# Kernel tuning notes

Hardware: AMD Instinct MI355X
Metric: run time of the kernel (lower is better)

Reference implementation:

```python
import jax, jax.numpy as jnp
import numpy as np
import math

IN_DIM = 512
LR_MUL = 1.0
SCALE = (1.0 / math.sqrt(IN_DIM)) * LR_MUL  # EqualLinear runtime weight scale


def setup_inputs() -> dict:
    key = jax.random.key(0)
    k1, k2 = jax.random.split(key)
    x = jax.random.normal(k1, (256, 18, 18, 512), dtype=jnp.float32)  # [B, n_out, n_layers, in_dim]
    W = jax.random.normal(k2, (18, 512, 512), dtype=jnp.float32)      # [n_out, out_dim, in_dim]
    b = jnp.zeros((18, 512), dtype=jnp.float32)                        # [n_out, out_dim], bias_init=0
    idx = jnp.arange(18, dtype=jnp.int32)                              # n_indx
    return {"x": x, "W": W, "b": b, "idx": idx}


def reference(x, W, b, idx):
    # Fused equivalent of the nested loops: for each direction i, apply
    # EqualLinear_i to slices x[:, i, j, :] for j in idx, writing results back.
    x_sel = x[:, :, idx, :]                                    # [B, O, J, D_in]
    y = jnp.einsum('koji,odi->kojd', x_sel, W) * SCALE         # [B, O, J, D_out]
    y = y + (b * LR_MUL)[None, :, None, :]
    return x.at[:, :, idx, :].set(y)
```

## Files before the change

kernel.cpp:

```cpp
#include <hip/hip_runtime.h>
#include <hip/hip_bf16.h>


typedef __bf16  bf16x8  __attribute__((ext_vector_type(8)));
typedef float   floatx4 __attribute__((ext_vector_type(4)));

#define O_DIM 18
#define J_DIM 18
#define KB    256
#define C_DIM 512
#define BM    128
#define BN    128
#define BK    32
#define NK    (C_DIM / BK)
#define LDSS  40

__device__ __forceinline__ __bf16 f2bf(float f) { return (__bf16)f; }

__device__ __forceinline__ void barrier_lds() {
    __builtin_amdgcn_s_waitcnt(0xc07f);
    __builtin_amdgcn_s_barrier();
}

__global__ __launch_bounds__(256, 2)
void dirnet_gemm(const float* __restrict__ x, const float* __restrict__ W,
                 const float* __restrict__ bias, const int* __restrict__ idx,
                 float* __restrict__ out)
{
    const int id   = blockIdx.x;
    const int xcd  = id & 7;
    const int slot = id >> 3;
    const int nt   = slot & 3;
    const int g    = (slot >> 2) * 8 + xcd;
    const int mt   = g & 1;
    const int jo   = g >> 1;
    const int j    = jo % J_DIM;
    const int o    = jo / J_DIM;
    const int jj   = idx[j];

    __shared__ __bf16 As[BM * LDSS];
    __shared__ __bf16 Bs[BN * LDSS];

    const int tid  = threadIdx.x;
    const int srow = tid >> 2;
    const int scol = (tid & 3) << 3;

    const float* xp = x + ((size_t)((mt * BM + srow) * O_DIM + o) * J_DIM + jj) * C_DIM + scol;
    const size_t xRS = (size_t)64 * O_DIM * J_DIM * C_DIM;
    const float* wp = W + ((size_t)(o * C_DIM + nt * BN + srow)) * C_DIM + scol;
    const size_t wRS = (size_t)64 * C_DIM;

    const int lane = tid & 63;
    const int wv   = tid >> 6;
    const int mOff = (wv & 1) * 64;
    const int nOff = (wv >> 1) * 64;
    const int lrow = lane & 15;
    const int lk   = (lane >> 4) << 3;

    floatx4 acc[4][4] = {};
    float4 pa[2][2][2];
    float4 pb[2][2];

    #pragma unroll
    for (int p = 0; p < 2; ++p) {
        pb[p][0] = *(const float4*)(wp + p * wRS);
        pb[p][1] = *(const float4*)(wp + p * wRS + 4);
    }
    #pragma unroll
    for (int p = 0; p < 2; ++p) {
        pa[0][p][0] = *(const float4*)(xp + p * xRS);
        pa[0][p][1] = *(const float4*)(xp + p * xRS + 4);
    }
    #pragma unroll
    for (int p = 0; p < 2; ++p) {
        pa[1][p][0] = *(const float4*)(xp + p * xRS + BK);
        pa[1][p][1] = *(const float4*)(xp + p * xRS + BK + 4);
    }

    #pragma unroll
    for (int t = 0; t < NK; ++t) {
        const int s = t & 1;

        bf16x8 sa[2], sb[2];
        #pragma unroll
        for (int p = 0; p < 2; ++p) {
            sa[p][0]=f2bf(pa[s][p][0].x); sa[p][1]=f2bf(pa[s][p][0].y);
            sa[p][2]=f2bf(pa[s][p][0].z); sa[p][3]=f2bf(pa[s][p][0].w);
            sa[p][4]=f2bf(pa[s][p][1].x); sa[p][5]=f2bf(pa[s][p][1].y);
            sa[p][6]=f2bf(pa[s][p][1].z); sa[p][7]=f2bf(pa[s][p][1].w);
        }
        #pragma unroll
        for (int p = 0; p < 2; ++p) {
            sb[p][0]=f2bf(pb[p][0].x); sb[p][1]=f2bf(pb[p][0].y);
            sb[p][2]=f2bf(pb[p][0].z); sb[p][3]=f2bf(pb[p][0].w);
            sb[p][4]=f2bf(pb[p][1].x); sb[p][5]=f2bf(pb[p][1].y);
            sb[p][6]=f2bf(pb[p][1].z); sb[p][7]=f2bf(pb[p][1].w);
        }

        barrier_lds();
        #pragma unroll
        for (int p = 0; p < 2; ++p) {
            *(bf16x8*)&As[(p * 64 + srow) * LDSS + scol] = sa[p];
            *(bf16x8*)&Bs[(p * 64 + srow) * LDSS + scol] = sb[p];
        }
        barrier_lds();

        if (t + 1 < NK) {
            const int k1 = (t + 1) * BK;
            #pragma unroll
            for (int p = 0; p < 2; ++p) {
                pb[p][0] = *(const float4*)(wp + p * wRS + k1);
                pb[p][1] = *(const float4*)(wp + p * wRS + k1 + 4);
            }
        }
        if (t + 2 < NK) {
            const int k2 = (t + 2) * BK;
            #pragma unroll
            for (int p = 0; p < 2; ++p) {
                pa[s][p][0] = *(const float4*)(xp + p * xRS + k2);
                pa[s][p][1] = *(const float4*)(xp + p * xRS + k2 + 4);
            }
        }

        bf16x8 af[4], bfr[4];
        #pragma unroll
        for (int mi = 0; mi < 4; ++mi)
            af[mi] = *(const bf16x8*)&As[(mOff + mi * 16 + lrow) * LDSS + lk];
        #pragma unroll
        for (int ni = 0; ni < 4; ++ni)
            bfr[ni] = *(const bf16x8*)&Bs[(nOff + ni * 16 + lrow) * LDSS + lk];

        #pragma unroll
        for (int mi = 0; mi < 4; ++mi)
            #pragma unroll
            for (int ni = 0; ni < 4; ++ni)
                acc[mi][ni] = __builtin_amdgcn_mfma_f32_16x16x32_bf16(
                    af[mi], bfr[ni], acc[mi][ni], 0, 0, 0);
    }

    const float scale = 0.04419417382415922f;
    const int rbase = (lane >> 4) << 2;
    #pragma unroll
    for (int ni = 0; ni < 4; ++ni) {
        const int d  = nt * BN + nOff + ni * 16 + lrow;
        const float bv = bias[o * C_DIM + d];
        #pragma unroll
        for (int mi = 0; mi < 4; ++mi) {
            #pragma unroll
            for (int r = 0; r < 4; ++r) {
                const int kr = mt * BM + mOff + mi * 16 + rbase + r;
                out[((size_t)(kr * O_DIM + o) * J_DIM + jj) * C_DIM + d] =
                    acc[mi][ni][r] * scale + bv;
            }
        }
    }
}

__global__ void copy_nonsel(const float* __restrict__ x, const int* __restrict__ idx,
                            float* __restrict__ out)
{
    const int jj = blockIdx.x;
    const int o  = blockIdx.y;
    bool member = false;
    for (int t = 0; t < J_DIM; ++t) member = member || (idx[t] == jj);
    if (member) return;
    const int tid = threadIdx.x;
    for (int k = 0; k < KB; ++k) {
        const size_t base = ((size_t)(k * O_DIM + o) * J_DIM + jj) * C_DIM;
        for (int c = tid * 4; c < C_DIM; c += 256 * 4) {
            *(float4*)&out[base + c] = *(const float4*)&x[base + c];
        }
    }
}

extern "C" void kernel_launch(void* const* d_in, const int* in_sizes, int n_in,
                              void* d_out, int out_size, void* d_ws, size_t ws_size,
                              hipStream_t stream) {
    const float* x   = (const float*)d_in[0];
    const float* W   = (const float*)d_in[1];
    const float* b   = (const float*)d_in[2];
    const int*   idx = (const int*)d_in[3];
    float* out = (float*)d_out;

    dirnet_gemm<<<dim3(2 * 4 * J_DIM * O_DIM), 256, 0, stream>>>(x, W, b, idx, out);
    copy_nonsel<<<dim3(J_DIM, O_DIM), 256, 0, stream>>>(x, idx, out);
}
```

Baseline: 366.4 us.

## Double-buffer W prefetch and remap blocks to contiguous per-XCD tile ranges

The W (B operand) register prefetch now uses two stages, matching the A operand, so both operands are loaded two K-steps ahead. The block-to-tile mapping is changed so each XCD gets a contiguous range of 81 (o, j, mt) groups, which keeps the W slices for a given o mostly on one XCD's L2. Compiler memory barriers are added around the LDS barrier. The deeper prefetch needs more registers, which could hurt occupancy under launch_bounds(256,2).

```diff
diff --git a/kernel.cpp b/kernel.cpp
--- a/kernel.cpp
+++ b/kernel.cpp
@@ -18,8 +18,10 @@
 __device__ __forceinline__ __bf16 f2bf(float f) { return (__bf16)f; }
 
 __device__ __forceinline__ void barrier_lds() {
+    asm volatile("" ::: "memory");
     __builtin_amdgcn_s_waitcnt(0xc07f);
     __builtin_amdgcn_s_barrier();
+    asm volatile("" ::: "memory");
 }
 
 __global__ __launch_bounds__(256, 2)
@@ -27,16 +29,17 @@
                  const float* __restrict__ bias, const int* __restrict__ idx,
                  float* __restrict__ out)
 {
-    const int id   = blockIdx.x;
-    const int xcd  = id & 7;
-    const int slot = id >> 3;
-    const int nt   = slot & 3;
-    const int g    = (slot >> 2) * 8 + xcd;
-    const int mt   = g & 1;
-    const int jo   = g >> 1;
-    const int j    = jo % J_DIM;
-    const int o    = jo / J_DIM;
-    const int jj   = idx[j];
+    const int id  = blockIdx.x;
+    const int xcd = id & 7;
+    const int r   = id >> 3;
+    const int nt  = r & 3;
+    const int q   = r >> 2;
+    const int T   = xcd * 81 + q;
+    const int o   = T / 36;
+    const int rem = T - o * 36;
+    const int j   = rem >> 1;
+    const int mt  = rem & 1;
+    const int jj  = idx[j];
 
     __shared__ __bf16 As[BM * LDSS];
     __shared__ __bf16 Bs[BN * LDSS];
@@ -59,67 +62,68 @@
 
     floatx4 acc[4][4] = {};
     float4 pa[2][2][2];
-    float4 pb[2][2];
+    float4 pb[2][2][2];
 
-    #pragma unroll
-    for (int p = 0; p < 2; ++p) {
-        pb[p][0] = *(const float4*)(wp + p * wRS);
-        pb[p][1] = *(const float4*)(wp + p * wRS + 4);
+#define LOAD_A(set, kk)                                                \
+    {                                                                  \
+        _Pragma("unroll")                                              \
+        for (int p = 0; p < 2; ++p) {                                  \
+            pa[set][p][0] = *(const float4*)(xp + p * xRS + (kk));     \
+            pa[set][p][1] = *(const float4*)(xp + p * xRS + (kk) + 4); \
+        }                                                              \
     }
-    #pragma unroll
-    for (int p = 0; p < 2; ++p) {
-        pa[0][p][0] = *(const float4*)(xp + p * xRS);
-        pa[0][p][1] = *(const float4*)(xp + p * xRS + 4);
+#define LOAD_B(set, kk)                                                \
+    {                                                                  \
+        _Pragma("unroll")                                              \
+        for (int p = 0; p < 2; ++p) {                                  \
+            pb[set][p][0] = *(const float4*)(wp + p * wRS + (kk));     \
+            pb[set][p][1] = *(const float4*)(wp + p * wRS + (kk) + 4); \
+        }                                                              \
     }
-    #pragma unroll
-    for (int p = 0; p < 2; ++p) {
-        pa[1][p][0] = *(const float4*)(xp + p * xRS + BK);
-        pa[1][p][1] = *(const float4*)(xp + p * xRS + BK + 4);
+#define CVT_AB(set, sa, sb)                                                   \
+    {                                                                         \
+        _Pragma("unroll")                                                     \
+        for (int p = 0; p < 2; ++p) {                                         \
+            sa[p][0]=f2bf(pa[set][p][0].x); sa[p][1]=f2bf(pa[set][p][0].y);   \
+            sa[p][2]=f2bf(pa[set][p][0].z); sa[p][3]=f2bf(pa[set][p][0].w);   \
+            sa[p][4]=f2bf(pa[set][p][1].x); sa[p][5]=f2bf(pa[set][p][1].y);   \
+            sa[p][6]=f2bf(pa[set][p][1].z); sa[p][7]=f2bf(pa[set][p][1].w);   \
+        }                                                                     \
+        _Pragma("unroll")                                                     \
+        for (int p = 0; p < 2; ++p) {                                         \
+            sb[p][0]=f2bf(pb[set][p][0].x); sb[p][1]=f2bf(pb[set][p][0].y);   \
+            sb[p][2]=f2bf(pb[set][p][0].z); sb[p][3]=f2bf(pb[set][p][0].w);   \
+            sb[p][4]=f2bf(pb[set][p][1].x); sb[p][5]=f2bf(pb[set][p][1].y);   \
+            sb[p][6]=f2bf(pb[set][p][1].z); sb[p][7]=f2bf(pb[set][p][1].w);   \
+        }                                                                     \
     }
+#define STORE_AB(sa, sb)                                               \
+    {                                                                  \
+        _Pragma("unroll")                                              \
+        for (int p = 0; p < 2; ++p) {                                  \
+            *(bf16x8*)&As[(p * 64 + srow) * LDSS + scol] = sa[p];      \
+            *(bf16x8*)&Bs[(p * 64 + srow) * LDSS + scol] = sb[p];      \
+        }                                                              \
+    }
+
+    LOAD_A(0, 0);       LOAD_B(0, 0);
+    LOAD_A(1, BK);      LOAD_B(1, BK);
 
     #pragma unroll
     for (int t = 0; t < NK; ++t) {
         const int s = t & 1;
 
         bf16x8 sa[2], sb[2];
-        #pragma unroll
-        for (int p = 0; p < 2; ++p) {
-            sa[p][0]=f2bf(pa[s][p][0].x); sa[p][1]=f2bf(pa[s][p][0].y);
-            sa[p][2]=f2bf(pa[s][p][0].z); sa[p][3]=f2bf(pa[s][p][0].w);
-            sa[p][4]=f2bf(pa[s][p][1].x); sa[p][5]=f2bf(pa[s][p][1].y);
-            sa[p][6]=f2bf(pa[s][p][1].z); sa[p][7]=f2bf(pa[s][p][1].w);
-        }
-        #pragma unroll
-        for (int p = 0; p < 2; ++p) {
-            sb[p][0]=f2bf(pb[p][0].x); sb[p][1]=f2bf(pb[p][0].y);
-            sb[p][2]=f2bf(pb[p][0].z); sb[p][3]=f2bf(pb[p][0].w);
-            sb[p][4]=f2bf(pb[p][1].x); sb[p][5]=f2bf(pb[p][1].y);
-            sb[p][6]=f2bf(pb[p][1].z); sb[p][7]=f2bf(pb[p][1].w);
-        }
+        CVT_AB(s, sa, sb);
 
         barrier_lds();
-        #pragma unroll
-        for (int p = 0; p < 2; ++p) {
-            *(bf16x8*)&As[(p * 64 + srow) * LDSS + scol] = sa[p];
-            *(bf16x8*)&Bs[(p * 64 + srow) * LDSS + scol] = sb[p];
-        }
+        STORE_AB(sa, sb);
         barrier_lds();
 
-        if (t + 1 < NK) {
-            const int k1 = (t + 1) * BK;
-            #pragma unroll
-            for (int p = 0; p < 2; ++p) {
-                pb[p][0] = *(const float4*)(wp + p * wRS + k1);
-                pb[p][1] = *(const float4*)(wp + p * wRS + k1 + 4);
-            }
-        }
         if (t + 2 < NK) {
             const int k2 = (t + 2) * BK;
-            #pragma unroll
-            for (int p = 0; p < 2; ++p) {
-                pa[s][p][0] = *(const float4*)(xp + p * xRS + k2);
-                pa[s][p][1] = *(const float4*)(xp + p * xRS + k2 + 4);
-            }
+            LOAD_A(s, k2);
+            LOAD_B(s, k2);
         }
 
         bf16x8 af[4], bfr[4];
@@ -138,6 +142,11 @@
                     af[mi], bfr[ni], acc[mi][ni], 0, 0, 0);
     }
 
+#undef LOAD_A
+#undef LOAD_B
+#undef CVT_AB
+#undef STORE_AB
+
     const float scale = 0.04419417382415922f;
     const int rbase = (lane >> 4) << 2;
     #pragma unroll
@@ -147,10 +156,10 @@
         #pragma unroll
         for (int mi = 0; mi < 4; ++mi) {
             #pragma unroll
-            for (int r = 0; r < 4; ++r) {
-                const int kr = mt * BM + mOff + mi * 16 + rbase + r;
+            for (int r2 = 0; r2 < 4; ++r2) {
+                const int kr = mt * BM + mOff + mi * 16 + rbase + r2;
                 out[((size_t)(kr * O_DIM + o) * J_DIM + jj) * C_DIM + d] =
-                    acc[mi][ni][r] * scale + bv;
+                    acc[mi][ni][r2] * scale + bv;
             }
         }
     }
```

Result: slower. 374.3 us (+2.2%).
